# Optimization experiments

Hardware: AMD Instinct MI355X
Metric: run time of the kernel (lower is better)

Reference implementation:

```python
import jax, jax.numpy as jnp
import numpy as np

B, T, C = 2, 2048, 2048
H, KVH, HD = 16, 4, 128
EPS = 1e-5


def _rope(x, cos, sin):
    # x: (B,T,h,HD); cos/sin: (1,T,1,HD//2); halves-split rotary (not interleaved)
    d = x.shape[-1] // 2
    x1, x2 = x[..., :d], x[..., d:]
    return jnp.concatenate([x1 * cos + x2 * sin, -x1 * sin + x2 * cos], axis=-1)


def _rms_norm(x, eps=EPS):
    return x * jax.lax.rsqrt(jnp.mean(x * x, axis=-1, keepdims=True) + eps)


def setup_inputs() -> dict:
    key = jax.random.key(0)
    ks = jax.random.split(key, 5)
    x = jax.random.normal(ks[0], (B, T, C), dtype=jnp.float32)
    # realistic RoPE tables (theta=10000)
    inv_freq = 1.0 / (10000.0 ** (np.arange(HD // 2, dtype=np.float32) / (HD // 2)))
    t = np.arange(T, dtype=np.float32)
    freqs = np.outer(t, inv_freq)  # (T, HD/2)
    cos = jnp.asarray(np.cos(freqs))[None, :, None, :]
    sin = jnp.asarray(np.sin(freqs))[None, :, None, :]
    s = 0.02
    wq = jax.random.normal(ks[1], (C, H * HD), dtype=jnp.float32) * s
    wk = jax.random.normal(ks[2], (C, KVH * HD), dtype=jnp.float32) * s
    wv = jax.random.normal(ks[3], (C, KVH * HD), dtype=jnp.float32) * s
    wo = jax.random.normal(ks[4], (H * HD, C), dtype=jnp.float32) * s
    return {"x": x, "cos": cos, "sin": sin, "wq": wq, "wk": wk, "wv": wv, "wo": wo, "window_size": 0}


def reference(x, cos, sin, wq, wk, wv, wo, window_size):
    # window_size is unused on the training (no-kv-cache) path, as in the source.
    b, t, _ = x.shape
    q = (x @ wq).reshape(b, t, H, HD)
    k = (x @ wk).reshape(b, t, KVH, HD)
    v = (x @ wv).reshape(b, t, KVH, HD)
    q = _rms_norm(_rope(q, cos, sin))
    k = _rms_norm(_rope(k, cos, sin))
    n_rep = H // KVH
    # grouped-query attention without materializing repeated K/V
    qg = q.reshape(b, t, KVH, n_rep, HD)
    scale = 1.0 / jnp.sqrt(jnp.float32(HD))
    scores = jnp.einsum('btkrd,bskd->bkrts', qg, k) * scale  # (B,KVH,n_rep,T,T)
    causal = jnp.tril(jnp.ones((t, t), dtype=bool))
    scores = jnp.where(causal, scores, jnp.finfo(scores.dtype).min)
    attn = jax.nn.softmax(scores, axis=-1)
    y = jnp.einsum('bkrts,bskd->btkrd', attn, v).reshape(b, t, H * HD)
    return y @ wo
```

## Files before the change

kernel.cpp:

```cpp
#include <hip/hip_runtime.h>
#include <hip/hip_bf16.h>


using bf16 = __bf16;
typedef __bf16 bf16x8 __attribute__((ext_vector_type(8)));
typedef __bf16 bf16x4 __attribute__((ext_vector_type(4)));
typedef float  f32x4  __attribute__((ext_vector_type(4)));

__device__ __forceinline__ void gload_lds16(const void* g, void* l) {
  __builtin_amdgcn_global_load_lds(
      (const __attribute__((address_space(1))) unsigned int*)g,
      (__attribute__((address_space(3))) unsigned int*)l, 16, 0, 0);
}

__device__ __forceinline__ unsigned pack2(float a, float b) {
  unsigned short ua = __builtin_bit_cast(unsigned short, (bf16)a);
  unsigned short ub = __builtin_bit_cast(unsigned short, (bf16)b);
  return ((unsigned)ub << 16) | ua;
}

__global__ __launch_bounds__(256) void k_cvt_bf16(const float* __restrict__ src,
                                                  bf16* __restrict__ dst) {
  const int i = blockIdx.x * 256 + threadIdx.x;
  f32x4 v = ((const f32x4*)src)[i];
  bf16x4 o;
  o[0] = (bf16)v[0]; o[1] = (bf16)v[1]; o[2] = (bf16)v[2]; o[3] = (bf16)v[3];
  ((bf16x4*)dst)[i] = o;
}

__global__ __launch_bounds__(256) void k_transpose_cvt(const float* __restrict__ src,
                                                       bf16* __restrict__ dst,
                                                       int R, int C) {
  __shared__ float tile[32][33];
  const int c0 = blockIdx.x * 32, r0 = blockIdx.y * 32;
  const int tx = threadIdx.x & 31, ty = threadIdx.x >> 5;
#pragma unroll
  for (int j = 0; j < 32; j += 8)
    tile[ty + j][tx] = src[(size_t)(r0 + ty + j) * C + c0 + tx];
  __syncthreads();
#pragma unroll
  for (int j = 0; j < 32; j += 8)
    dst[(size_t)(c0 + ty + j) * R + r0 + tx] = (bf16)tile[tx][ty + j];
}

template <bool OUT_BF16>
__global__ __launch_bounds__(256) void k_gemm(
    const bf16* __restrict__ A,
    const bf16* __restrict__ B0, const bf16* __restrict__ B1,
    const bf16* __restrict__ B2, int nb1, int nb2,
    void* __restrict__ Cout, int K, int Ntot) {
  __shared__ __align__(16) bf16 As[128 * 64];
  __shared__ __align__(16) bf16 Bs[128 * 64];
  const int nb = blockIdx.x, mb = blockIdx.y;
  const bf16* Bt; int nloc;
  if (nb < nb1)      { Bt = B0; nloc = nb; }
  else if (nb < nb2) { Bt = B1; nloc = nb - nb1; }
  else               { Bt = B2; nloc = nb - nb2; }
  const int tid = threadIdx.x;
  const int w = tid >> 6, lane = tid & 63;
  const int wm = w >> 1, wn = w & 1;
  const int sr = lane >> 3, sc = lane & 7;
  const int l16 = lane & 15, lq = lane >> 4;
  f32x4 acc[4][4] = {};
  const bf16* Ab = A  + (size_t)(mb * 128) * K;
  const bf16* Bb = Bt + (size_t)(nloc * 128) * K;
  for (int k0 = 0; k0 < K; k0 += 64) {
#pragma unroll
    for (int it = 0; it < 4; ++it) {
      const int r  = w * 32 + it * 8 + sr;
      const int cs = (sc ^ (r & 7)) << 3;
      gload_lds16(Ab + (size_t)r * K + k0 + cs, &As[(w * 32 + it * 8) * 64]);
      gload_lds16(Bb + (size_t)r * K + k0 + cs, &Bs[(w * 32 + it * 8) * 64]);
    }
    __syncthreads();
#pragma unroll
    for (int kc = 0; kc < 2; ++kc) {
      bf16x8 af[4], bfr[4];
#pragma unroll
      for (int i = 0; i < 4; ++i) {
        const int ra = wm * 64 + i * 16 + l16;
        af[i]  = *(const bf16x8*)((const char*)As + ra * 128 +
                                  ((kc * 64 + lq * 16) ^ ((ra & 7) << 4)));
        const int rb = wn * 64 + i * 16 + l16;
        bfr[i] = *(const bf16x8*)((const char*)Bs + rb * 128 +
                                  ((kc * 64 + lq * 16) ^ ((rb & 7) << 4)));
      }
#pragma unroll
      for (int i = 0; i < 4; ++i)
#pragma unroll
        for (int j = 0; j < 4; ++j)
          acc[i][j] = __builtin_amdgcn_mfma_f32_16x16x32_bf16(af[i], bfr[j],
                                                              acc[i][j], 0, 0, 0);
    }
    __syncthreads();
  }
#pragma unroll
  for (int i = 0; i < 4; ++i)
#pragma unroll
    for (int j = 0; j < 4; ++j)
#pragma unroll
      for (int e = 0; e < 4; ++e) {
        const size_t row = (size_t)mb * 128 + wm * 64 + i * 16 + lq * 4 + e;
        const size_t col = (size_t)nb * 128 + wn * 64 + j * 16 + l16;
        if (OUT_BF16) ((bf16*)Cout)[row * Ntot + col] = (bf16)acc[i][j][e];
        else          ((float*)Cout)[row * Ntot + col] = acc[i][j][e];
      }
}

__global__ __launch_bounds__(256) void k_rope(
    const bf16* __restrict__ qkv, const float* __restrict__ cosb,
    const float* __restrict__ sinb, bf16* __restrict__ q_r,
    bf16* __restrict__ k_r, bf16* __restrict__ v_t) {
  const int wid  = blockIdx.x * 4 + (threadIdx.x >> 6);
  const int lane = threadIdx.x & 63;
  const int head = wid % 24;
  const int bt   = wid / 24;
  const int b = bt >> 11, t = bt & 2047;
  const bf16* base = qkv + (size_t)bt * 3072;
  if (head >= 20) {
    const int kv = head - 20;
    const bf16 v1 = base[2560 + kv * 128 + lane];
    const bf16 v2 = base[2560 + kv * 128 + 64 + lane];
    const size_t o = (size_t)((b * 4 + kv) * 128);
    v_t[(o + lane) * 2048 + t]      = v1;
    v_t[(o + 64 + lane) * 2048 + t] = v2;
    return;
  }
  const int col = (head < 16) ? head * 128 : 2048 + (head - 16) * 128;
  const float x1 = (float)base[col + lane];
  const float x2 = (float)base[col + 64 + lane];
  const float c = cosb[t * 64 + lane], s = sinb[t * 64 + lane];
  const float o1 = x1 * c + x2 * s;
  const float o2 = x2 * c - x1 * s;
  float ss = o1 * o1 + o2 * o2;
#pragma unroll
  for (int off = 32; off >= 1; off >>= 1) ss += __shfl_xor(ss, off);
  float r = rsqrtf(ss * (1.0f / 128.0f) + 1e-5f);
  if (head < 16) {
    r *= 0.08838834764831845f;
    const size_t o = ((size_t)(b * 16 + head) * 2048 + t) * 128;
    q_r[o + lane]      = (bf16)(o1 * r);
    q_r[o + 64 + lane] = (bf16)(o2 * r);
  } else {
    const int kv = head - 16;
    const size_t o = ((size_t)(b * 4 + kv) * 2048 + t) * 128;
    k_r[o + lane]      = (bf16)(o1 * r);
    k_r[o + 64 + lane] = (bf16)(o2 * r);
  }
}

__global__ __launch_bounds__(256, 2) void k_attn(
    const bf16* __restrict__ q_r, const bf16* __restrict__ k_r,
    const bf16* __restrict__ v_t, bf16* __restrict__ y) {
  __shared__ __align__(16) bf16 Ks[2][64 * 128];
  __shared__ __align__(16) bf16 Vt[2][128 * 64];
  const int blkid = blockIdx.x;
  const int bh = (blkid & 7) * 4 + ((blkid >> 3) & 3);
  const int g  = blkid >> 5;
  const int qb = (blkid < 256) ? (15 - g) : (g - 8);
  const int b = bh >> 4, h = bh & 15;
  const int bkv = b * 4 + (h >> 2);
  const int tid = threadIdx.x, w = tid >> 6, lane = tid & 63;
  const int l16 = lane & 15, lq = lane >> 4;
  const int swz = (l16 & 7) << 4;
  const int q0 = qb * 128, t0A = q0 + w * 32;
  const int nt = 2 * qb + 2;
  const bf16* kb = k_r + (size_t)bkv * (2048 * 128);
  const bf16* vb = v_t + (size_t)bkv * (128 * 2048);

  bf16x8 qfA[4], qfB[4];
  const bf16* qbase = q_r + ((size_t)bh * 2048 + t0A + l16) * 128;
#pragma unroll
  for (int kc = 0; kc < 4; ++kc) {
    qfA[kc] = *(const bf16x8*)(qbase + 32 * kc + 8 * lq);
    qfB[kc] = *(const bf16x8*)(qbase + 16 * 128 + 32 * kc + 8 * lq);
  }

  f32x4 accA[8] = {}, accB[8] = {};
  float mA = -1e29f, mB = -1e29f, lA = 0.f, lB = 0.f;

  auto stage = [&](int buf, int s0n) {
#pragma unroll
    for (int it = 0; it < 4; ++it) {
      const int rK = w * 16 + it * 4 + (lane >> 4);
      gload_lds16(kb + (size_t)(s0n + rK) * 128 + (((lane & 15) ^ (rK & 7)) << 3),
                  &Ks[buf][(w * 16 + it * 4) * 128]);
      const int rV = w * 32 + it * 8 + (lane >> 3);
      gload_lds16(vb + (size_t)rV * 2048 + s0n + (((lane & 7) ^ (rV & 7)) << 3),
                  &Vt[buf][(w * 32 + it * 8) * 64]);
    }
  };

  stage(0, 0);
  asm volatile("s_waitcnt vmcnt(0)" ::: "memory");
  __syncthreads();

  for (int t = 0; t < nt; ++t) {
    if (t + 1 < nt) stage((t + 1) & 1, (t + 1) * 64);
    const int s0 = t * 64;
    const int buf = t & 1;
    if (s0 <= t0A + 31) {
      f32x4 stA[4] = {}, stB[4] = {};
#pragma unroll
      for (int kc = 0; kc < 4; ++kc)
#pragma unroll
        for (int n = 0; n < 4; ++n) {
          const int rk = 16 * n + l16;
          const bf16x8 kf = *(const bf16x8*)((const char*)&Ks[buf][0] +
                             rk * 256 + ((64 * kc + 16 * lq) ^ swz));
          stA[n] = __builtin_amdgcn_mfma_f32_16x16x32_bf16(kf, qfA[kc], stA[n], 0, 0, 0);
          stB[n] = __builtin_amdgcn_mfma_f32_16x16x32_bf16(kf, qfB[kc], stB[n], 0, 0, 0);
        }
      const int qgA = t0A + l16, qgB = qgA + 16;
      if (s0 + 63 > t0A) {
#pragma unroll
        for (int n = 0; n < 4; ++n)
#pragma unroll
          for (int e = 0; e < 4; ++e) {
            const int kvg = s0 + 16 * n + 4 * lq + e;
            if (kvg > qgA) stA[n][e] = -1e30f;
            if (kvg > qgB) stB[n][e] = -1e30f;
          }
      }
      float mxA = -1e30f, mxB = -1e30f;
#pragma unroll
      for (int n = 0; n < 4; ++n)
#pragma unroll
        for (int e = 0; e < 4; ++e) {
          mxA = fmaxf(mxA, stA[n][e]);
          mxB = fmaxf(mxB, stB[n][e]);
        }
      mxA = fmaxf(mxA, __shfl_xor(mxA, 16)); mxA = fmaxf(mxA, __shfl_xor(mxA, 32));
      mxB = fmaxf(mxB, __shfl_xor(mxB, 16)); mxB = fmaxf(mxB, __shfl_xor(mxB, 32));
      const bool small = (mxA <= mA + 8.f) && (mxB <= mB + 8.f);
      if (!__all(small)) {
        const float mnA = fmaxf(mA, mxA), mnB = fmaxf(mB, mxB);
        const float scA = __expf(mA - mnA), scB = __expf(mB - mnB);
        mA = mnA; mB = mnB; lA *= scA; lB *= scB;
#pragma unroll
        for (int d2 = 0; d2 < 8; ++d2) { accA[d2] *= scA; accB[d2] *= scB; }
      }
      float rsA = 0.f, rsB = 0.f;
#pragma unroll
      for (int n = 0; n < 4; ++n)
#pragma unroll
        for (int e = 0; e < 4; ++e) {
          stA[n][e] = __expf(stA[n][e] - mA); rsA += stA[n][e];
          stB[n][e] = __expf(stB[n][e] - mB); rsB += stB[n][e];
        }
      rsA += __shfl_xor(rsA, 16); rsA += __shfl_xor(rsA, 32); lA += rsA;
      rsB += __shfl_xor(rsB, 16); rsB += __shfl_xor(rsB, 32); lB += rsB;
      unsigned pA2[8], pB2[8];
#pragma unroll
      for (int n = 0; n < 4; ++n) {
        pA2[n * 2 + 0] = pack2(stA[n][0], stA[n][1]);
        pA2[n * 2 + 1] = pack2(stA[n][2], stA[n][3]);
        pB2[n * 2 + 0] = pack2(stB[n][0], stB[n][1]);
        pB2[n * 2 + 1] = pack2(stB[n][2], stB[n][3]);
      }
      const int src0 = l16 | ((((lq & 1) << 1) | 0) << 4);
      const int src1 = l16 | ((((lq & 1) << 1) | 1) << 4);
      const bool selhi = (lq & 2);
#pragma unroll
      for (int c = 0; c < 2; ++c) {
        union { unsigned u[4]; bf16x8 v; } wA, wB;
        {
          unsigned a0 = __shfl((int)pA2[(2*c)*2+0], src0), b0 = __shfl((int)pA2[(2*c+1)*2+0], src0);
          unsigned a1 = __shfl((int)pA2[(2*c)*2+1], src0), b1 = __shfl((int)pA2[(2*c+1)*2+1], src0);
          unsigned a2 = __shfl((int)pA2[(2*c)*2+0], src1), b2 = __shfl((int)pA2[(2*c+1)*2+0], src1);
          unsigned a3 = __shfl((int)pA2[(2*c)*2+1], src1), b3 = __shfl((int)pA2[(2*c+1)*2+1], src1);
          wA.u[0] = selhi ? b0 : a0; wA.u[1] = selhi ? b1 : a1;
          wA.u[2] = selhi ? b2 : a2; wA.u[3] = selhi ? b3 : a3;
        }
        {
          unsigned a0 = __shfl((int)pB2[(2*c)*2+0], src0), b0 = __shfl((int)pB2[(2*c+1)*2+0], src0);
          unsigned a1 = __shfl((int)pB2[(2*c)*2+1], src0), b1 = __shfl((int)pB2[(2*c+1)*2+1], src0);
          unsigned a2 = __shfl((int)pB2[(2*c)*2+0], src1), b2 = __shfl((int)pB2[(2*c+1)*2+0], src1);
          unsigned a3 = __shfl((int)pB2[(2*c)*2+1], src1), b3 = __shfl((int)pB2[(2*c+1)*2+1], src1);
          wB.u[0] = selhi ? b0 : a0; wB.u[1] = selhi ? b1 : a1;
          wB.u[2] = selhi ? b2 : a2; wB.u[3] = selhi ? b3 : a3;
        }
#pragma unroll
        for (int dblk = 0; dblk < 8; ++dblk) {
          const int rv = 16 * dblk + l16;
          const bf16x8 vf = *(const bf16x8*)((const char*)&Vt[buf][0] +
                             rv * 128 + ((64 * c + 16 * lq) ^ swz));
          accA[dblk] = __builtin_amdgcn_mfma_f32_16x16x32_bf16(vf, wA.v, accA[dblk], 0, 0, 0);
          accB[dblk] = __builtin_amdgcn_mfma_f32_16x16x32_bf16(vf, wB.v, accB[dblk], 0, 0, 0);
        }
      }
    }
    asm volatile("s_waitcnt vmcnt(0)" ::: "memory");
    __syncthreads();
  }

  const float invA = 1.f / lA, invB = 1.f / lB;
  bf16* yA = y + (((size_t)b * 2048 + t0A + l16) * 16 + h) * 128;
  bf16* yB = yA + (size_t)16 * 2048;
#pragma unroll
  for (int dblk = 0; dblk < 8; ++dblk) {
    unsigned loA = pack2(accA[dblk][0] * invA, accA[dblk][1] * invA);
    unsigned hiA = pack2(accA[dblk][2] * invA, accA[dblk][3] * invA);
    *(uint2*)(yA + 16 * dblk + 4 * lq) = make_uint2(loA, hiA);
    unsigned loB = pack2(accB[dblk][0] * invB, accB[dblk][1] * invB);
    unsigned hiB = pack2(accB[dblk][2] * invB, accB[dblk][3] * invB);
    *(uint2*)(yB + 16 * dblk + 4 * lq) = make_uint2(loB, hiB);
  }
}

extern "C" void kernel_launch(void* const* d_in, const int* in_sizes, int n_in,
                              void* d_out, int out_size, void* d_ws, size_t ws_size,
                              hipStream_t stream) {
  const float* x    = (const float*)d_in[0];
  const float* cosb = (const float*)d_in[1];
  const float* sinb = (const float*)d_in[2];
  const float* wq   = (const float*)d_in[3];
  const float* wk   = (const float*)d_in[4];
  const float* wv   = (const float*)d_in[5];
  const float* wo   = (const float*)d_in[6];
  float* out = (float*)d_out;

  char* ws = (char*)d_ws;
  size_t off = 0;
  auto alloc = [&](size_t bytes) {
    char* p = ws + off; off += (bytes + 255) & ~(size_t)255; return p;
  };
  bf16* xb  = (bf16*)alloc(4096ull * 2048 * 2);
  bf16* wqT = (bf16*)alloc(2048ull * 2048 * 2);
  bf16* wkT = (bf16*)alloc(512ull  * 2048 * 2);
  bf16* wvT = (bf16*)alloc(512ull  * 2048 * 2);
  bf16* woT = (bf16*)alloc(2048ull * 2048 * 2);
  bf16* qkv = (bf16*)alloc(4096ull * 3072 * 2);
  bf16* q_r = (bf16*)alloc(4096ull * 2048 * 2);
  bf16* k_r = (bf16*)alloc(4096ull * 512  * 2);
  bf16* v_t = (bf16*)alloc(4096ull * 512  * 2);
  bf16* y   = xb;

  k_cvt_bf16<<<(4096 * 2048 / 4) / 256, 256, 0, stream>>>(x, xb);
  k_transpose_cvt<<<dim3(64, 64), 256, 0, stream>>>(wq, wqT, 2048, 2048);
  k_transpose_cvt<<<dim3(16, 64), 256, 0, stream>>>(wk, wkT, 2048, 512);
  k_transpose_cvt<<<dim3(16, 64), 256, 0, stream>>>(wv, wvT, 2048, 512);
  k_transpose_cvt<<<dim3(64, 64), 256, 0, stream>>>(wo, woT, 2048, 2048);
  k_gemm<true><<<dim3(24, 32), 256, 0, stream>>>(xb, wqT, wkT, wvT, 16, 20,
                                                 qkv, 2048, 3072);
  k_rope<<<24576, 256, 0, stream>>>(qkv, cosb, sinb, q_r, k_r, v_t);
  k_attn<<<512, 256, 0, stream>>>(q_r, k_r, v_t, y);
  k_gemm<false><<<dim3(16, 32), 256, 0, stream>>>(y, woT, woT, woT, 100, 200,
                                                  out, 2048, 2048);
}
```

Before: 335.7 us.

## Replace GEMM with 8-wave double-buffered kernel using larger tiles

Swaps the 128x128 single-buffered GEMM for a 512-thread kernel with 256-wide N tiles and BM of 256 (QKV) or 128 (output projection). Global-to-LDS loads for the next K-step are double-buffered and interleaved with MFMA phases, with explicit barriers, waitcnts and setprio. The aim is to hide load latency and raise data reuse per tile. In exchange it uses fewer blocks (192 and 256 on the grid), which may leave CUs underfilled, and adds more LDS use and register pressure.

After: 380.9 us. 1.13x slower.

```diff
diff --git a/kernel.cpp b/kernel.cpp
--- a/kernel.cpp
+++ b/kernel.cpp
@@ -18,6 +18,11 @@
   unsigned short ub = __builtin_bit_cast(unsigned short, (bf16)b);
   return ((unsigned)ub << 16) | ua;
 }
+
+#define SBAR() __builtin_amdgcn_s_barrier()
+#define WAIT_LGKM0() do { asm volatile("s_waitcnt lgkmcnt(0)" ::: "memory"); \
+                          __builtin_amdgcn_sched_barrier(0); } while (0)
+#define WAIT_VM0() asm volatile("s_waitcnt vmcnt(0)" ::: "memory")
 
 __global__ __launch_bounds__(256) void k_cvt_bf16(const float* __restrict__ src,
                                                   bf16* __restrict__ dst) {
@@ -43,14 +48,17 @@
     dst[(size_t)(c0 + ty + j) * R + r0 + tx] = (bf16)tile[tx][ty + j];
 }
 
-template <bool OUT_BF16>
-__global__ __launch_bounds__(256) void k_gemm(
+template <int BM, bool OUT_BF16>
+__global__ __launch_bounds__(512, 2) void k_gemm8(
     const bf16* __restrict__ A,
     const bf16* __restrict__ B0, const bf16* __restrict__ B1,
     const bf16* __restrict__ B2, int nb1, int nb2,
     void* __restrict__ Cout, int K, int Ntot) {
-  __shared__ __align__(16) bf16 As[128 * 64];
-  __shared__ __align__(16) bf16 Bs[128 * 64];
+  constexpr int MR  = BM / 32;
+  constexpr int RPP = MR / 4;
+  constexpr int ACH = BM / 64;
+  __shared__ __align__(16) bf16 As[2][BM * 64];
+  __shared__ __align__(16) bf16 Bs[2][256 * 64];
   const int nb = blockIdx.x, mb = blockIdx.y;
   const bf16* Bt; int nloc;
   if (nb < nb1)      { Bt = B0; nloc = nb; }
@@ -58,50 +66,97 @@
   else               { Bt = B2; nloc = nb - nb2; }
   const int tid = threadIdx.x;
   const int w = tid >> 6, lane = tid & 63;
-  const int wm = w >> 1, wn = w & 1;
-  const int sr = lane >> 3, sc = lane & 7;
+  const int wm = w >> 2, wn = w & 3;
   const int l16 = lane & 15, lq = lane >> 4;
-  f32x4 acc[4][4] = {};
-  const bf16* Ab = A  + (size_t)(mb * 128) * K;
-  const bf16* Bb = Bt + (size_t)(nloc * 128) * K;
-  for (int k0 = 0; k0 < K; k0 += 64) {
-#pragma unroll
-    for (int it = 0; it < 4; ++it) {
-      const int r  = w * 32 + it * 8 + sr;
-      const int cs = (sc ^ (r & 7)) << 3;
-      gload_lds16(Ab + (size_t)r * K + k0 + cs, &As[(w * 32 + it * 8) * 64]);
-      gload_lds16(Bb + (size_t)r * K + k0 + cs, &Bs[(w * 32 + it * 8) * 64]);
+  const int r8 = lane >> 3, c8 = lane & 7;
+  const bf16* Ag = A  + (size_t)mb * BM * K;
+  const bf16* Bg = Bt + (size_t)nloc * 256 * K;
+
+  f32x4 acc[MR][4] = {};
+
+  auto stageA = [&](int bn, int k0, int ch) {
+    const int r = ch * 64 + w * 8 + r8;
+    gload_lds16(Ag + (size_t)r * K + k0 + ((c8 ^ (r & 7)) << 3),
+                &As[bn][(ch * 64 + w * 8) * 64]);
+  };
+  auto stageB = [&](int bn, int k0, int ch) {
+    const int r = ch * 64 + w * 8 + r8;
+    gload_lds16(Bg + (size_t)r * K + k0 + ((c8 ^ (r & 7)) << 3),
+                &Bs[bn][(ch * 64 + w * 8) * 64]);
+  };
+
+#pragma unroll
+  for (int ch = 0; ch < ACH; ++ch) stageA(0, 0, ch);
+#pragma unroll
+  for (int ch = 0; ch < 4; ++ch) stageB(0, 0, ch);
+  WAIT_VM0();
+  SBAR();
+
+  const int NT = K / 64;
+  bf16x8 bfr[4][2];
+  for (int t = 0; t < NT; ++t) {
+    const int buf = t & 1;
+    const int k0n = (t + 1) * 64;
+    const bool pf = (t + 1 < NT);
+#pragma unroll
+    for (int p = 0; p < 4; ++p) {
+      if (pf) {
+        if (p == 0) {
+          stageB(buf ^ 1, k0n, 0); stageB(buf ^ 1, k0n, 1);
+          stageA(buf ^ 1, k0n, 0);
+          if (ACH > 1) stageA(buf ^ 1, k0n, 1);
+        } else if (p == 1) {
+          stageB(buf ^ 1, k0n, 2);
+          if (ACH > 2) stageA(buf ^ 1, k0n, 2);
+        } else if (p == 2) {
+          stageB(buf ^ 1, k0n, 3);
+          if (ACH > 3) stageA(buf ^ 1, k0n, 3);
+        }
+      }
+      if (p == 0) {
+#pragma unroll
+        for (int j = 0; j < 4; ++j)
+#pragma unroll
+          for (int kc = 0; kc < 2; ++kc) {
+            const int rb = wn * 64 + j * 16 + l16;
+            bfr[j][kc] = *(const bf16x8*)((const char*)&Bs[buf][0] +
+                          rb * 128 + ((kc * 64 + lq * 16) ^ ((rb & 7) << 4)));
+          }
+      }
+      bf16x8 af[RPP][2];
+#pragma unroll
+      for (int ii = 0; ii < RPP; ++ii)
+#pragma unroll
+        for (int kc = 0; kc < 2; ++kc) {
+          const int ra = wm * (BM / 2) + (p * RPP + ii) * 16 + l16;
+          af[ii][kc] = *(const bf16x8*)((const char*)&As[buf][0] +
+                        ra * 128 + ((kc * 64 + lq * 16) ^ ((ra & 7) << 4)));
+        }
+      SBAR();
+      WAIT_LGKM0();
+      __builtin_amdgcn_s_setprio(1);
+#pragma unroll
+      for (int kc = 0; kc < 2; ++kc)
+#pragma unroll
+        for (int ii = 0; ii < RPP; ++ii)
+#pragma unroll
+          for (int j = 0; j < 4; ++j)
+            acc[p * RPP + ii][j] = __builtin_amdgcn_mfma_f32_16x16x32_bf16(
+                af[ii][kc], bfr[j][kc], acc[p * RPP + ii][j], 0, 0, 0);
+      __builtin_amdgcn_s_setprio(0);
+      if (p == 3 && pf) WAIT_VM0();
+      SBAR();
     }
-    __syncthreads();
-#pragma unroll
-    for (int kc = 0; kc < 2; ++kc) {
-      bf16x8 af[4], bfr[4];
-#pragma unroll
-      for (int i = 0; i < 4; ++i) {
-        const int ra = wm * 64 + i * 16 + l16;
-        af[i]  = *(const bf16x8*)((const char*)As + ra * 128 +
-                                  ((kc * 64 + lq * 16) ^ ((ra & 7) << 4)));
-        const int rb = wn * 64 + i * 16 + l16;
-        bfr[i] = *(const bf16x8*)((const char*)Bs + rb * 128 +
-                                  ((kc * 64 + lq * 16) ^ ((rb & 7) << 4)));
-      }
-#pragma unroll
-      for (int i = 0; i < 4; ++i)
-#pragma unroll
-        for (int j = 0; j < 4; ++j)
-          acc[i][j] = __builtin_amdgcn_mfma_f32_16x16x32_bf16(af[i], bfr[j],
-                                                              acc[i][j], 0, 0, 0);
-    }
-    __syncthreads();
-  }
-#pragma unroll
-  for (int i = 0; i < 4; ++i)
+  }
+
+#pragma unroll
+  for (int i = 0; i < MR; ++i)
 #pragma unroll
     for (int j = 0; j < 4; ++j)
 #pragma unroll
       for (int e = 0; e < 4; ++e) {
-        const size_t row = (size_t)mb * 128 + wm * 64 + i * 16 + lq * 4 + e;
-        const size_t col = (size_t)nb * 128 + wn * 64 + j * 16 + l16;
+        const size_t row = (size_t)mb * BM + wm * (BM / 2) + i * 16 + lq * 4 + e;
+        const size_t col = (size_t)nb * 256 + wn * 64 + j * 16 + l16;
         if (OUT_BF16) ((bf16*)Cout)[row * Ntot + col] = (bf16)acc[i][j][e];
         else          ((float*)Cout)[row * Ntot + col] = acc[i][j][e];
       }
@@ -341,10 +396,10 @@
   k_transpose_cvt<<<dim3(16, 64), 256, 0, stream>>>(wk, wkT, 2048, 512);
   k_transpose_cvt<<<dim3(16, 64), 256, 0, stream>>>(wv, wvT, 2048, 512);
   k_transpose_cvt<<<dim3(64, 64), 256, 0, stream>>>(wo, woT, 2048, 2048);
-  k_gemm<true><<<dim3(24, 32), 256, 0, stream>>>(xb, wqT, wkT, wvT, 16, 20,
-                                                 qkv, 2048, 3072);
+  k_gemm8<256, true><<<dim3(12, 16), 512, 0, stream>>>(xb, wqT, wkT, wvT, 8, 10,
+                                                       qkv, 2048, 3072);
   k_rope<<<24576, 256, 0, stream>>>(qkv, cosb, sinb, q_r, k_r, v_t);
   k_attn<<<512, 256, 0, stream>>>(q_r, k_r, v_t, y);
-  k_gemm<false><<<dim3(16, 32), 256, 0, stream>>>(y, woT, woT, woT, 100, 200,
-                                                  out, 2048, 2048);
-}
+  k_gemm8<128, false><<<dim3(8, 32), 512, 0, stream>>>(y, woT, woT, woT, 100, 200,
+                                                       out, 2048, 2048);
+}
```

## Rewrite projection GEMMs with larger tiles and 4-stage async LDS pipeline

Applied to the files above, without the earlier changes.

Replaces the 128x128 single-buffered GEMM with a 512-thread kernel using 256-wide N tiles (BM=256 for QKV, 128 for output) and a 4-deep ring of LDS buffers. Loads run three stages ahead, with explicit vmcnt waits and s_setprio around the MFMA block. The goal is to overlap global-to-LDS traffic with MFMA work and improve operand reuse per tile. In exchange the grids shrink to 192 and 256 blocks on a GPU with many CUs, so occupancy and wave balance may suffer, and LDS use per block is higher.

Result: slower. 364.6 us (+8.6%).

```diff
diff --git a/kernel.cpp b/kernel.cpp
--- a/kernel.cpp
+++ b/kernel.cpp
@@ -18,6 +18,10 @@
   unsigned short ub = __builtin_bit_cast(unsigned short, (bf16)b);
   return ((unsigned)ub << 16) | ua;
 }
+
+#define SBAR() do { __builtin_amdgcn_s_barrier(); \
+                    __builtin_amdgcn_sched_barrier(0); } while (0)
+#define VMCNT(n) asm volatile("s_waitcnt vmcnt(" #n ")" ::: "memory")
 
 __global__ __launch_bounds__(256) void k_cvt_bf16(const float* __restrict__ src,
                                                   bf16* __restrict__ dst) {
@@ -43,14 +47,16 @@
     dst[(size_t)(c0 + ty + j) * R + r0 + tx] = (bf16)tile[tx][ty + j];
 }
 
-template <bool OUT_BF16>
-__global__ __launch_bounds__(256) void k_gemm(
+template <int BM, bool OUT_BF16>
+__global__ __launch_bounds__(512, 1) void k_gemm32(
     const bf16* __restrict__ A,
     const bf16* __restrict__ B0, const bf16* __restrict__ B1,
     const bf16* __restrict__ B2, int nb1, int nb2,
     void* __restrict__ Cout, int K, int Ntot) {
-  __shared__ __align__(16) bf16 As[128 * 64];
-  __shared__ __align__(16) bf16 Bs[128 * 64];
+  constexpr int MR  = BM / 32;
+  constexpr int ACH = BM / 128;
+  __shared__ __align__(16) bf16 As[4][BM * 32];
+  __shared__ __align__(16) bf16 Bs[4][256 * 32];
   const int nb = blockIdx.x, mb = blockIdx.y;
   const bf16* Bt; int nloc;
   if (nb < nb1)      { Bt = B0; nloc = nb; }
@@ -58,50 +64,86 @@
   else               { Bt = B2; nloc = nb - nb2; }
   const int tid = threadIdx.x;
   const int w = tid >> 6, lane = tid & 63;
-  const int wm = w >> 1, wn = w & 1;
-  const int sr = lane >> 3, sc = lane & 7;
+  const int wm = w >> 2, wn = w & 3;
   const int l16 = lane & 15, lq = lane >> 4;
-  f32x4 acc[4][4] = {};
-  const bf16* Ab = A  + (size_t)(mb * 128) * K;
-  const bf16* Bb = Bt + (size_t)(nloc * 128) * K;
-  for (int k0 = 0; k0 < K; k0 += 64) {
-#pragma unroll
-    for (int it = 0; it < 4; ++it) {
-      const int r  = w * 32 + it * 8 + sr;
-      const int cs = (sc ^ (r & 7)) << 3;
-      gload_lds16(Ab + (size_t)r * K + k0 + cs, &As[(w * 32 + it * 8) * 64]);
-      gload_lds16(Bb + (size_t)r * K + k0 + cs, &Bs[(w * 32 + it * 8) * 64]);
-    }
-    __syncthreads();
-#pragma unroll
-    for (int kc = 0; kc < 2; ++kc) {
-      bf16x8 af[4], bfr[4];
-#pragma unroll
-      for (int i = 0; i < 4; ++i) {
-        const int ra = wm * 64 + i * 16 + l16;
-        af[i]  = *(const bf16x8*)((const char*)As + ra * 128 +
-                                  ((kc * 64 + lq * 16) ^ ((ra & 7) << 4)));
-        const int rb = wn * 64 + i * 16 + l16;
-        bfr[i] = *(const bf16x8*)((const char*)Bs + rb * 128 +
-                                  ((kc * 64 + lq * 16) ^ ((rb & 7) << 4)));
-      }
-#pragma unroll
-      for (int i = 0; i < 4; ++i)
-#pragma unroll
-        for (int j = 0; j < 4; ++j)
-          acc[i][j] = __builtin_amdgcn_mfma_f32_16x16x32_bf16(af[i], bfr[j],
-                                                              acc[i][j], 0, 0, 0);
-    }
-    __syncthreads();
-  }
-#pragma unroll
-  for (int i = 0; i < 4; ++i)
+  const int sr4 = lane >> 2, sc4 = lane & 3;
+  const bf16* Ag = A  + (size_t)mb * BM * K;
+  const bf16* Bg = Bt + (size_t)nloc * 256 * K;
+
+  f32x4 acc[MR][4] = {};
+
+  auto stage = [&](int t) {
+    const int buf = t & 3;
+    const int k0 = t * 32;
+#pragma unroll
+    for (int i = 0; i < 2; ++i) {
+      const int r = i * 128 + w * 16 + sr4;
+      const int cg = sc4 ^ ((r >> 1) & 3);
+      gload_lds16(Bg + (size_t)r * K + k0 + cg * 8,
+                  &Bs[buf][(i * 128 + w * 16) * 32]);
+    }
+#pragma unroll
+    for (int i = 0; i < ACH; ++i) {
+      const int r = i * 128 + w * 16 + sr4;
+      const int cg = sc4 ^ ((r >> 1) & 3);
+      gload_lds16(Ag + (size_t)r * K + k0 + cg * 8,
+                  &As[buf][(i * 128 + w * 16) * 32]);
+    }
+  };
+
+  const int NT = K / 32;
+  stage(0); stage(1); stage(2);
+  if (BM == 256) VMCNT(8); else VMCNT(6);
+  SBAR();
+
+  for (int t = 0; t < NT; ++t) {
+    const int buf = t & 3;
+    if (t + 3 < NT) stage(t + 3);
+    const int rem = NT - 1 - t;
+    if (BM == 256) {
+      if (rem >= 3)      VMCNT(12);
+      else if (rem == 2) VMCNT(8);
+      else if (rem == 1) VMCNT(4);
+      else               VMCNT(0);
+    } else {
+      if (rem >= 3)      VMCNT(9);
+      else if (rem == 2) VMCNT(6);
+      else if (rem == 1) VMCNT(3);
+      else               VMCNT(0);
+    }
+    SBAR();
+    bf16x8 bfr[4], af[MR];
+#pragma unroll
+    for (int j = 0; j < 4; ++j) {
+      const int rb = wn * 64 + j * 16 + l16;
+      bfr[j] = *(const bf16x8*)((const char*)&Bs[buf][0] + rb * 64 +
+                                ((lq ^ ((rb >> 1) & 3)) << 4));
+    }
+#pragma unroll
+    for (int i = 0; i < MR; ++i) {
+      const int ra = wm * (BM / 2) + i * 16 + l16;
+      af[i] = *(const bf16x8*)((const char*)&As[buf][0] + ra * 64 +
+                               ((lq ^ ((ra >> 1) & 3)) << 4));
+    }
+    __builtin_amdgcn_s_setprio(1);
+#pragma unroll
+    for (int i = 0; i < MR; ++i)
+#pragma unroll
+      for (int j = 0; j < 4; ++j)
+        acc[i][j] = __builtin_amdgcn_mfma_f32_16x16x32_bf16(af[i], bfr[j],
+                                                            acc[i][j], 0, 0, 0);
+    __builtin_amdgcn_s_setprio(0);
+    SBAR();
+  }
+
+#pragma unroll
+  for (int i = 0; i < MR; ++i)
 #pragma unroll
     for (int j = 0; j < 4; ++j)
 #pragma unroll
       for (int e = 0; e < 4; ++e) {
-        const size_t row = (size_t)mb * 128 + wm * 64 + i * 16 + lq * 4 + e;
-        const size_t col = (size_t)nb * 128 + wn * 64 + j * 16 + l16;
+        const size_t row = (size_t)mb * BM + wm * (BM / 2) + i * 16 + lq * 4 + e;
+        const size_t col = (size_t)nb * 256 + wn * 64 + j * 16 + l16;
         if (OUT_BF16) ((bf16*)Cout)[row * Ntot + col] = (bf16)acc[i][j][e];
         else          ((float*)Cout)[row * Ntot + col] = acc[i][j][e];
       }
@@ -341,10 +383,10 @@
   k_transpose_cvt<<<dim3(16, 64), 256, 0, stream>>>(wk, wkT, 2048, 512);
   k_transpose_cvt<<<dim3(16, 64), 256, 0, stream>>>(wv, wvT, 2048, 512);
   k_transpose_cvt<<<dim3(64, 64), 256, 0, stream>>>(wo, woT, 2048, 2048);
-  k_gemm<true><<<dim3(24, 32), 256, 0, stream>>>(xb, wqT, wkT, wvT, 16, 20,
-                                                 qkv, 2048, 3072);
+  k_gemm32<256, true><<<dim3(12, 16), 512, 0, stream>>>(xb, wqT, wkT, wvT, 8, 10,
+                                                        qkv, 2048, 3072);
   k_rope<<<24576, 256, 0, stream>>>(qkv, cosb, sinb, q_r, k_r, v_t);
   k_attn<<<512, 256, 0, stream>>>(q_r, k_r, v_t, y);
-  k_gemm<false><<<dim3(16, 32), 256, 0, stream>>>(y, woT, woT, woT, 100, 200,
-                                                  out, 2048, 2048);
-}
+  k_gemm32<128, false><<<dim3(8, 32), 512, 0, stream>>>(y, woT, woT, woT, 100, 200,
+                                                        out, 2048, 2048);
+}
```
